# Kernel tuning notes

Measured on AMD Instinct MI355X. Metric: run time of the kernel, lower is better.

The kernel has to match this reference:

```python
import jax, jax.numpy as jnp
import numpy as np

N_NODES = 50000
N_EDGES = 600000
D = 128
LN_EPS = 1e-5


def _mlp_ln(x, W1, b1, W2, b2, g, beta):
    # Linear -> ReLU -> Linear -> LayerNorm (standard MeshGraphNets model_fn)
    h = jax.nn.relu(x @ W1 + b1)
    y = h @ W2 + b2
    mu = jnp.mean(y, axis=-1, keepdims=True)
    var = jnp.var(y, axis=-1, keepdims=True)
    return (y - mu) * jax.lax.rsqrt(var + LN_EPS) * g + beta


def setup_inputs() -> dict:
    key = jax.random.key(0)
    ks = jax.random.split(key, 16)
    def glorot(k, shape):
        fan = shape[0] + shape[1]
        return jax.random.normal(k, shape, jnp.float32) * np.sqrt(2.0 / fan)
    inp = {
        "node_features": jax.random.normal(ks[0], (1, N_NODES, D), jnp.float32),
        "edge_features": jax.random.normal(ks[1], (1, N_EDGES, D), jnp.float32),
        "senders": jax.random.randint(ks[2], (N_EDGES,), 0, N_NODES),
        "receivers": jax.random.randint(ks[3], (N_EDGES,), 0, N_NODES),
        # edge MLP: in 3*D -> 128 -> D, LayerNorm
        "eW1": glorot(ks[4], (3 * D, 128)), "eb1": jnp.zeros((128,), jnp.float32),
        "eW2": glorot(ks[5], (128, D)), "eb2": jnp.zeros((D,), jnp.float32),
        "eg": jnp.ones((D,), jnp.float32), "ebeta": jnp.zeros((D,), jnp.float32),
        # node MLP: in 2*D -> 128 -> D, LayerNorm
        "nW1": glorot(ks[6], (2 * D, 128)), "nb1": jnp.zeros((128,), jnp.float32),
        "nW2": glorot(ks[7], (128, D)), "nb2": jnp.zeros((D,), jnp.float32),
        "ng": jnp.ones((D,), jnp.float32), "nbeta": jnp.zeros((D,), jnp.float32),
        # attention linear D -> 1
        "aW": glorot(ks[8], (D, 1)), "ab": jnp.zeros((1,), jnp.float32),
    }
    return inp


def reference(node_features, edge_features, senders, receivers,
              eW1, eb1, eW2, eb2, eg, ebeta,
              nW1, nb1, nW2, nb2, ng, nbeta,
              aW, ab):
    # --- edge update: gather + concat + MLP ---
    sf = node_features[:, senders]      # [1,E,D]
    rf = node_features[:, receivers]    # [1,E,D]
    new_ef = _mlp_ln(jnp.concatenate([sf, rf, edge_features], -1),
                     eW1, eb1, eW2, eb2, eg, ebeta)  # [1,E,D]
    # --- per-edge attention: linear + LeakyReLU + scatter_softmax over receivers ---
    logits = jax.nn.leaky_relu(new_ef @ aW + ab, 0.2)[0, :, 0]  # [E]
    seg_max = jax.ops.segment_max(logits, receivers, num_segments=N_NODES)
    seg_max = jnp.where(jnp.isfinite(seg_max), seg_max, 0.0)
    ex = jnp.exp(logits - seg_max[receivers])
    seg_sum = jax.ops.segment_sum(ex, receivers, num_segments=N_NODES)
    att = ex / seg_sum[receivers]  # [E]
    # --- scatter-add aggregation ---
    agg = jax.ops.segment_sum(new_ef[0] * att[:, None], receivers,
                              num_segments=N_NODES)[None]  # [1,N,D]
    new_nf = _mlp_ln(jnp.concatenate([node_features, agg], -1),
                     nW1, nb1, nW2, nb2, ng, nbeta)  # [1,N,D]
    # residual connections
    new_nf = new_nf + node_features
    new_ef = new_ef + edge_features
    return new_nf, new_ef
```

## Files before the change

### kernel.cpp

```cpp
#include <hip/hip_runtime.h>
#include <hip/hip_bf16.h>

#define N_NODES 50000
#define N_EDGES 600000
#define D 128
#define LN_EPS 1e-5f

typedef float f32x4 __attribute__((ext_vector_type(4)));
typedef int   i32x4 __attribute__((ext_vector_type(4)));
typedef short s16x8 __attribute__((ext_vector_type(8)));

#define W1P_OFF     0u
#define W2P_OFF     98304u
#define NW1P_OFF    131072u
#define NW2P_OFF    196608u
#define SEGKEY_OFF  229376u
#define SEGSUM_OFF  429440u
#define LOGITS_OFF  629504u
#define EX_OFF      3029504u
#define AGG_OFF     5429504u

static __device__ __forceinline__ unsigned short f2bf(float f) {
    unsigned int u = __float_as_uint(f);
    u = (u + 0x7FFFu + ((u >> 16) & 1u)) >> 16;
    return (unsigned short)u;
}
static __device__ __forceinline__ int pkbf2(float a, float b) {
    union { __hip_bfloat16 h[2]; int i; } u;
    u.h[0] = __float2bfloat16(a);
    u.h[1] = __float2bfloat16(b);
    return u.i;
}
union frag_u { i32x4 i; s16x8 s; };
static __device__ __forceinline__ unsigned int fkey(float f) {
    unsigned int u = __float_as_uint(f);
    return (u & 0x80000000u) ? ~u : (u | 0x80000000u);
}
static __device__ __forceinline__ float unkey(unsigned int k) {
    unsigned int u = (k & 0x80000000u) ? (k & 0x7FFFFFFFu) : ~k;
    return __uint_as_float(u);
}
static __device__ __forceinline__ f32x4 mfma_bf16(s16x8 a, s16x8 b, f32x4 c) {
    return __builtin_amdgcn_mfma_f32_16x16x32_bf16(a, b, c, 0, 0, 0);
}

__global__ void k_init(const float* __restrict__ eW1, const float* __restrict__ eW2,
                       const float* __restrict__ nW1, const float* __restrict__ nW2,
                       char* __restrict__ ws) {
    int idx = blockIdx.x * 256 + threadIdx.x;
    if (idx < N_NODES * D) ((float*)(ws + AGG_OFF))[idx] = 0.0f;
    if (idx < N_NODES) {
        ((unsigned int*)(ws + SEGKEY_OFF))[idx] = 0u;
        ((float*)(ws + SEGSUM_OFF))[idx] = 0.0f;
    }
    int e = idx & 7, lane = (idx >> 3) & 63, ct = (idx >> 9) & 7, ks = idx >> 12;
    int k = ks * 32 + (lane >> 4) * 8 + e;
    int j = ct * 16 + (lane & 15);
    if (idx < 12 * 4096) ((unsigned short*)(ws + W1P_OFF))[idx]  = f2bf(eW1[k * 128 + j]);
    if (idx < 4 * 4096)  ((unsigned short*)(ws + W2P_OFF))[idx]  = f2bf(eW2[k * 128 + j]);
    if (idx < 8 * 4096)  ((unsigned short*)(ws + NW1P_OFF))[idx] = f2bf(nW1[k * 128 + j]);
    if (idx < 4 * 4096)  ((unsigned short*)(ws + NW2P_OFF))[idx] = f2bf(nW2[k * 128 + j]);
}

__global__ __launch_bounds__(256, 4) void k_edge(
    const float* __restrict__ nf, const float* __restrict__ ef,
    const int* __restrict__ snd, const int* __restrict__ rcv,
    const s16x8* __restrict__ B1, const s16x8* __restrict__ B2,
    const float* __restrict__ b1, const float* __restrict__ b2,
    const float* __restrict__ g, const float* __restrict__ beta,
    const float* __restrict__ aW, const float* __restrict__ ab,
    float* __restrict__ out_ef, float* __restrict__ logits,
    unsigned int* __restrict__ segkey)
{
    __shared__ __align__(16) char hbuf[64 * 128 * 2];
    const int tid = threadIdx.x, lane = tid & 63, rt = tid >> 6;
    const int j0 = lane & 15, hi = lane >> 4;

    const long eA = (long)blockIdx.x * 64 + rt * 16 + j0;
    const int sA = snd[eA], rA = rcv[eA];
    const float* __restrict__ prowS = nf + (size_t)sA * D;
    const float* __restrict__ prowR = nf + (size_t)rA * D;
    const float* __restrict__ prowE = ef + (size_t)eA * D;

    f32x4 acc[8];
    #pragma unroll
    for (int ct = 0; ct < 8; ++ct) acc[ct] = (f32x4){0.f, 0.f, 0.f, 0.f};
    #pragma unroll
    for (int ks = 0; ks < 12; ++ks) {
        const float* p = (ks < 4 ? prowS : (ks < 8 ? prowR : prowE)) + (ks & 3) * 32 + hi * 8;
        float4 f0 = *(const float4*)p;
        float4 f1 = *(const float4*)(p + 4);
        frag_u a;
        a.i[0] = pkbf2(f0.x, f0.y); a.i[1] = pkbf2(f0.z, f0.w);
        a.i[2] = pkbf2(f1.x, f1.y); a.i[3] = pkbf2(f1.z, f1.w);
        #pragma unroll
        for (int ct = 0; ct < 8; ++ct)
            acc[ct] = mfma_bf16(a.s, B1[(ks * 8 + ct) * 64 + lane], acc[ct]);
    }

    #pragma unroll
    for (int ct = 0; ct < 8; ++ct) {
        float bb = b1[ct * 16 + j0];
        #pragma unroll
        for (int rg = 0; rg < 4; ++rg) {
            int row = rt * 16 + hi * 4 + rg;
            float y = fmaxf(acc[ct][rg] + bb, 0.0f);
            int addr = (row * 256 + (ct * 16 + j0) * 2) ^ ((row & 7) << 4);
            *(__hip_bfloat16*)(hbuf + addr) = __float2bfloat16(y);
        }
    }
    asm volatile("" ::: "memory");

    f32x4 acc2[8];
    #pragma unroll
    for (int ct = 0; ct < 8; ++ct) acc2[ct] = (f32x4){0.f, 0.f, 0.f, 0.f};
    {
        int arow = rt * 16 + j0;
        #pragma unroll
        for (int ks = 0; ks < 4; ++ks) {
            int addr = (arow * 256 + (ks * 32 + hi * 8) * 2) ^ ((arow & 7) << 4);
            frag_u a;
            a.i = *(const i32x4*)(hbuf + addr);
            #pragma unroll
            for (int ct = 0; ct < 8; ++ct)
                acc2[ct] = mfma_bf16(a.s, B2[(ks * 8 + ct) * 64 + lane], acc2[ct]);
        }
    }

    float b2v[8], gv[8], bv[8], awv[8];
    #pragma unroll
    for (int ct = 0; ct < 8; ++ct) {
        int c = ct * 16 + j0;
        b2v[ct] = b2[c]; gv[ct] = g[c]; bv[ct] = beta[c]; awv[ct] = aW[c];
    }
    float abv = ab[0];
    #pragma unroll
    for (int rg = 0; rg < 4; ++rg) {
        int row = rt * 16 + hi * 4 + rg;
        long e = (long)blockIdx.x * 64 + row;
        float y[8]; float s = 0.f, sq = 0.f;
        #pragma unroll
        for (int ct = 0; ct < 8; ++ct) {
            y[ct] = acc2[ct][rg] + b2v[ct];
            s += y[ct]; sq += y[ct] * y[ct];
        }
        #pragma unroll
        for (int m = 1; m <= 8; m <<= 1) { s += __shfl_xor(s, m); sq += __shfl_xor(sq, m); }
        float mu = s * (1.0f / 128.0f);
        float var = sq * (1.0f / 128.0f) - mu * mu;
        float rs = rsqrtf(var + LN_EPS);
        const float* efr = ef + (size_t)e * D;
        float* outr = out_ef + (size_t)e * D;
        float lg = 0.f;
        #pragma unroll
        for (int ct = 0; ct < 8; ++ct) {
            int c = ct * 16 + j0;
            float o = (y[ct] - mu) * rs * gv[ct] + bv[ct];
            outr[c] = o + efr[c];
            lg += o * awv[ct];
        }
        #pragma unroll
        for (int m = 1; m <= 8; m <<= 1) lg += __shfl_xor(lg, m);
        if (j0 == 0) {
            float L = lg + abv;
            L = (L >= 0.f) ? L : 0.2f * L;
            logits[e] = L;
            atomicMax(&segkey[rcv[e]], fkey(L));
        }
    }
}

__global__ void k_exps(const float* __restrict__ logits, const int* __restrict__ rcv,
                       const unsigned int* __restrict__ segkey,
                       float* __restrict__ ex, float* __restrict__ segsum)
{
    int e = blockIdx.x * 256 + threadIdx.x;
    if (e >= N_EDGES) return;
    int r = rcv[e];
    float v = __expf(logits[e] - unkey(segkey[r]));
    ex[e] = v;
    unsafeAtomicAdd(&segsum[r], v);
}

__global__ void k_scatter(const float* __restrict__ out_ef, const float* __restrict__ ef,
                          const int* __restrict__ rcv, const float* __restrict__ ex,
                          const float* __restrict__ segsum, float* __restrict__ agg)
{
    long idx = (long)blockIdx.x * 256 + threadIdx.x;
    int e = (int)(idx >> 7);
    int c = (int)(idx & 127);
    int r = rcv[e];
    float att = ex[e] / segsum[r];
    float raw = out_ef[idx] - ef[idx];
    unsafeAtomicAdd(&agg[(size_t)r * D + c], raw * att);
}

__global__ __launch_bounds__(256, 4) void k_node(
    const float* __restrict__ nf, const float* __restrict__ agg,
    const s16x8* __restrict__ B1, const s16x8* __restrict__ B2,
    const float* __restrict__ b1, const float* __restrict__ b2,
    const float* __restrict__ g, const float* __restrict__ beta,
    float* __restrict__ out_nf)
{
    __shared__ __align__(16) char hbuf[64 * 128 * 2];
    const int tid = threadIdx.x, lane = tid & 63, rt = tid >> 6;
    const int j0 = lane & 15, hi = lane >> 4;

    long nA = (long)blockIdx.x * 64 + rt * 16 + j0;
    if (nA >= N_NODES) nA = 0;
    const float* __restrict__ prowN = nf  + (size_t)nA * D;
    const float* __restrict__ prowA = agg + (size_t)nA * D;

    f32x4 acc[8];
    #pragma unroll
    for (int ct = 0; ct < 8; ++ct) acc[ct] = (f32x4){0.f, 0.f, 0.f, 0.f};
    #pragma unroll
    for (int ks = 0; ks < 8; ++ks) {
        const float* p = (ks < 4 ? prowN : prowA) + (ks & 3) * 32 + hi * 8;
        float4 f0 = *(const float4*)p;
        float4 f1 = *(const float4*)(p + 4);
        frag_u a;
        a.i[0] = pkbf2(f0.x, f0.y); a.i[1] = pkbf2(f0.z, f0.w);
        a.i[2] = pkbf2(f1.x, f1.y); a.i[3] = pkbf2(f1.z, f1.w);
        #pragma unroll
        for (int ct = 0; ct < 8; ++ct)
            acc[ct] = mfma_bf16(a.s, B1[(ks * 8 + ct) * 64 + lane], acc[ct]);
    }

    #pragma unroll
    for (int ct = 0; ct < 8; ++ct) {
        float bb = b1[ct * 16 + j0];
        #pragma unroll
        for (int rg = 0; rg < 4; ++rg) {
            int row = rt * 16 + hi * 4 + rg;
            float y = fmaxf(acc[ct][rg] + bb, 0.0f);
            int addr = (row * 256 + (ct * 16 + j0) * 2) ^ ((row & 7) << 4);
            *(__hip_bfloat16*)(hbuf + addr) = __float2bfloat16(y);
        }
    }
    asm volatile("" ::: "memory");

    f32x4 acc2[8];
    #pragma unroll
    for (int ct = 0; ct < 8; ++ct) acc2[ct] = (f32x4){0.f, 0.f, 0.f, 0.f};
    {
        int arow = rt * 16 + j0;
        #pragma unroll
        for (int ks = 0; ks < 4; ++ks) {
            int addr = (arow * 256 + (ks * 32 + hi * 8) * 2) ^ ((arow & 7) << 4);
            frag_u a;
            a.i = *(const i32x4*)(hbuf + addr);
            #pragma unroll
            for (int ct = 0; ct < 8; ++ct)
                acc2[ct] = mfma_bf16(a.s, B2[(ks * 8 + ct) * 64 + lane], acc2[ct]);
        }
    }

    float b2v[8], gv[8], bv[8];
    #pragma unroll
    for (int ct = 0; ct < 8; ++ct) {
        int c = ct * 16 + j0;
        b2v[ct] = b2[c]; gv[ct] = g[c]; bv[ct] = beta[c];
    }
    #pragma unroll
    for (int rg = 0; rg < 4; ++rg) {
        int row = rt * 16 + hi * 4 + rg;
        long n = (long)blockIdx.x * 64 + row;
        float y[8]; float s = 0.f, sq = 0.f;
        #pragma unroll
        for (int ct = 0; ct < 8; ++ct) {
            y[ct] = acc2[ct][rg] + b2v[ct];
            s += y[ct]; sq += y[ct] * y[ct];
        }
        #pragma unroll
        for (int m = 1; m <= 8; m <<= 1) { s += __shfl_xor(s, m); sq += __shfl_xor(sq, m); }
        float mu = s * (1.0f / 128.0f);
        float var = sq * (1.0f / 128.0f) - mu * mu;
        float rs = rsqrtf(var + LN_EPS);
        if (n < N_NODES) {
            const float* nfr = nf + (size_t)n * D;
            float* outr = out_nf + (size_t)n * D;
            #pragma unroll
            for (int ct = 0; ct < 8; ++ct) {
                int c = ct * 16 + j0;
                float o = (y[ct] - mu) * rs * gv[ct] + bv[ct];
                outr[c] = o + nfr[c];
            }
        }
    }
}

extern "C" void kernel_launch(void* const* d_in, const int* in_sizes, int n_in,
                              void* d_out, int out_size, void* d_ws, size_t ws_size,
                              hipStream_t stream)
{
    (void)in_sizes; (void)n_in; (void)out_size; (void)ws_size;
    const float* nf    = (const float*)d_in[0];
    const float* ef    = (const float*)d_in[1];
    const int*   snd   = (const int*)d_in[2];
    const int*   rcv   = (const int*)d_in[3];
    const float* eW1   = (const float*)d_in[4];
    const float* eb1   = (const float*)d_in[5];
    const float* eW2   = (const float*)d_in[6];
    const float* eb2   = (const float*)d_in[7];
    const float* eg    = (const float*)d_in[8];
    const float* ebeta = (const float*)d_in[9];
    const float* nW1   = (const float*)d_in[10];
    const float* nb1   = (const float*)d_in[11];
    const float* nW2   = (const float*)d_in[12];
    const float* nb2   = (const float*)d_in[13];
    const float* ng    = (const float*)d_in[14];
    const float* nbeta = (const float*)d_in[15];
    const float* aW    = (const float*)d_in[16];
    const float* ab    = (const float*)d_in[17];

    float* out_nf = (float*)d_out;
    float* out_ef = out_nf + (size_t)N_NODES * D;
    char*  ws     = (char*)d_ws;

    k_init<<<25000, 256, 0, stream>>>(eW1, eW2, nW1, nW2, ws);

    k_edge<<<N_EDGES / 64, 256, 0, stream>>>(
        nf, ef, snd, rcv,
        (const s16x8*)(ws + W1P_OFF), (const s16x8*)(ws + W2P_OFF),
        eb1, eb2, eg, ebeta, aW, ab,
        out_ef, (float*)(ws + LOGITS_OFF), (unsigned int*)(ws + SEGKEY_OFF));

    k_exps<<<(N_EDGES + 255) / 256, 256, 0, stream>>>(
        (const float*)(ws + LOGITS_OFF), rcv, (const unsigned int*)(ws + SEGKEY_OFF),
        (float*)(ws + EX_OFF), (float*)(ws + SEGSUM_OFF));

    k_scatter<<<(int)(((long)N_EDGES * D) / 256), 256, 0, stream>>>(
        out_ef, ef, rcv, (const float*)(ws + EX_OFF),
        (const float*)(ws + SEGSUM_OFF), (float*)(ws + AGG_OFF));

    k_node<<<(N_NODES + 63) / 64, 256, 0, stream>>>(
        nf, (const float*)(ws + AGG_OFF),
        (const s16x8*)(ws + NW1P_OFF), (const s16x8*)(ws + NW2P_OFF),
        nb1, nb2, ng, nbeta, out_nf);
}
```

Baseline: 728.5 us.

## Stage edge-MLP weight fragments through double-buffered LDS in k_edge

Before, each of the 4 waves in k_edge read weight fragments straight from global memory for every MFMA. Now the block cooperatively copies each 8KB k-slice of W1, then W2, into a double-buffered LDS area while the current slice is consumed, with a __syncthreads per step. The goal is to cut redundant global and L2 weight traffic and the register pressure from loading B fragments inline, and acc2 is folded into acc to free registers. In exchange it adds 16 KB of LDS per block, which may limit occupancy, plus a barrier every k-step.

```diff
diff --git a/kernel.cpp b/kernel.cpp
--- a/kernel.cpp
+++ b/kernel.cpp
@@ -65,14 +65,15 @@
 __global__ __launch_bounds__(256, 4) void k_edge(
     const float* __restrict__ nf, const float* __restrict__ ef,
     const int* __restrict__ snd, const int* __restrict__ rcv,
-    const s16x8* __restrict__ B1, const s16x8* __restrict__ B2,
+    const i32x4* __restrict__ B1, const i32x4* __restrict__ B2,
     const float* __restrict__ b1, const float* __restrict__ b2,
     const float* __restrict__ g, const float* __restrict__ beta,
     const float* __restrict__ aW, const float* __restrict__ ab,
     float* __restrict__ out_ef, float* __restrict__ logits,
     unsigned int* __restrict__ segkey)
 {
-    __shared__ __align__(16) char hbuf[64 * 128 * 2];
+    __shared__ __align__(16) char  hbuf[64 * 128 * 2];
+    __shared__ __align__(16) i32x4 bstage[2][512];
     const int tid = threadIdx.x, lane = tid & 63, rt = tid >> 6;
     const int j0 = lane & 15, hi = lane >> 4;
 
@@ -82,20 +83,31 @@
     const float* __restrict__ prowR = nf + (size_t)rA * D;
     const float* __restrict__ prowE = ef + (size_t)eA * D;
 
+    bstage[0][2 * tid]     = B1[2 * tid];
+    bstage[0][2 * tid + 1] = B1[2 * tid + 1];
+    __syncthreads();
+
     f32x4 acc[8];
     #pragma unroll
     for (int ct = 0; ct < 8; ++ct) acc[ct] = (f32x4){0.f, 0.f, 0.f, 0.f};
-    #pragma unroll
-    for (int ks = 0; ks < 12; ++ks) {
-        const float* p = (ks < 4 ? prowS : (ks < 8 ? prowR : prowE)) + (ks & 3) * 32 + hi * 8;
+    for (int s = 0; s < 12; ++s) {
+        const int cur = s & 1, nxt = cur ^ 1;
+        const i32x4* src = (s + 1 < 12) ? (B1 + (s + 1) * 512) : (B2 + (s + 1 - 12) * 512);
+        i32x4 t0 = src[2 * tid], t1 = src[2 * tid + 1];
+        bstage[nxt][2 * tid]     = t0;
+        bstage[nxt][2 * tid + 1] = t1;
+        const float* p = (s < 4 ? prowS : (s < 8 ? prowR : prowE)) + (s & 3) * 32 + hi * 8;
         float4 f0 = *(const float4*)p;
         float4 f1 = *(const float4*)(p + 4);
         frag_u a;
         a.i[0] = pkbf2(f0.x, f0.y); a.i[1] = pkbf2(f0.z, f0.w);
         a.i[2] = pkbf2(f1.x, f1.y); a.i[3] = pkbf2(f1.z, f1.w);
         #pragma unroll
-        for (int ct = 0; ct < 8; ++ct)
-            acc[ct] = mfma_bf16(a.s, B1[(ks * 8 + ct) * 64 + lane], acc[ct]);
+        for (int ct = 0; ct < 8; ++ct) {
+            frag_u b; b.i = bstage[cur][ct * 64 + lane];
+            acc[ct] = mfma_bf16(a.s, b.s, acc[ct]);
+        }
+        __syncthreads();
     }
 
     #pragma unroll
@@ -111,19 +123,27 @@
     }
     asm volatile("" ::: "memory");
 
-    f32x4 acc2[8];
-    #pragma unroll
-    for (int ct = 0; ct < 8; ++ct) acc2[ct] = (f32x4){0.f, 0.f, 0.f, 0.f};
+    #pragma unroll
+    for (int ct = 0; ct < 8; ++ct) acc[ct] = (f32x4){0.f, 0.f, 0.f, 0.f};
     {
-        int arow = rt * 16 + j0;
-        #pragma unroll
-        for (int ks = 0; ks < 4; ++ks) {
-            int addr = (arow * 256 + (ks * 32 + hi * 8) * 2) ^ ((arow & 7) << 4);
+        const int arow = rt * 16 + j0;
+        for (int s2 = 0; s2 < 4; ++s2) {
+            const int s = 12 + s2, cur = s & 1, nxt = cur ^ 1;
+            if (s2 < 3) {
+                const i32x4* src = B2 + (s2 + 1) * 512;
+                i32x4 t0 = src[2 * tid], t1 = src[2 * tid + 1];
+                bstage[nxt][2 * tid]     = t0;
+                bstage[nxt][2 * tid + 1] = t1;
+            }
+            int addr = (arow * 256 + (s2 * 32 + hi * 8) * 2) ^ ((arow & 7) << 4);
             frag_u a;
             a.i = *(const i32x4*)(hbuf + addr);
             #pragma unroll
-            for (int ct = 0; ct < 8; ++ct)
-                acc2[ct] = mfma_bf16(a.s, B2[(ks * 8 + ct) * 64 + lane], acc2[ct]);
+            for (int ct = 0; ct < 8; ++ct) {
+                frag_u b; b.i = bstage[cur][ct * 64 + lane];
+                acc[ct] = mfma_bf16(a.s, b.s, acc[ct]);
+            }
+            if (s2 < 3) __syncthreads();
         }
     }
 
@@ -141,7 +161,7 @@
         float y[8]; float s = 0.f, sq = 0.f;
         #pragma unroll
         for (int ct = 0; ct < 8; ++ct) {
-            y[ct] = acc2[ct][rg] + b2v[ct];
+            y[ct] = acc[ct][rg] + b2v[ct];
             s += y[ct]; sq += y[ct] * y[ct];
         }
         #pragma unroll
@@ -240,9 +260,8 @@
     }
     asm volatile("" ::: "memory");
 
-    f32x4 acc2[8];
-    #pragma unroll
-    for (int ct = 0; ct < 8; ++ct) acc2[ct] = (f32x4){0.f, 0.f, 0.f, 0.f};
+    #pragma unroll
+    for (int ct = 0; ct < 8; ++ct) acc[ct] = (f32x4){0.f, 0.f, 0.f, 0.f};
     {
         int arow = rt * 16 + j0;
         #pragma unroll
@@ -252,7 +271,7 @@
             a.i = *(const i32x4*)(hbuf + addr);
             #pragma unroll
             for (int ct = 0; ct < 8; ++ct)
-                acc2[ct] = mfma_bf16(a.s, B2[(ks * 8 + ct) * 64 + lane], acc2[ct]);
+                acc[ct] = mfma_bf16(a.s, B2[(ks * 8 + ct) * 64 + lane], acc[ct]);
         }
     }
 
@@ -269,7 +288,7 @@
         float y[8]; float s = 0.f, sq = 0.f;
         #pragma unroll
         for (int ct = 0; ct < 8; ++ct) {
-            y[ct] = acc2[ct][rg] + b2v[ct];
+            y[ct] = acc[ct][rg] + b2v[ct];
             s += y[ct]; sq += y[ct] * y[ct];
         }
         #pragma unroll
@@ -322,7 +341,7 @@
 
     k_edge<<<N_EDGES / 64, 256, 0, stream>>>(
         nf, ef, snd, rcv,
-        (const s16x8*)(ws + W1P_OFF), (const s16x8*)(ws + W2P_OFF),
+        (const i32x4*)(ws + W1P_OFF), (const i32x4*)(ws + W2P_OFF),
         eb1, eb2, eg, ebeta, aW, ab,
         out_ef, (float*)(ws + LOGITS_OFF), (unsigned int*)(ws + SEGKEY_OFF));
 
```

Result: faster. 633.1 us (-13.1%).
